# Performance work log

Hardware: AMD Instinct MI355X
Metric: run time of the kernel (lower is better)

The kernel has to match this reference:

```python
import jax, jax.numpy as jnp
import numpy as np

SCALE = 0.08838834764831845  # 1/sqrt(128)

def setup_inputs() -> dict:
    key = jax.random.key(0)
    k1, k2 = jax.random.split(key)
    x1 = jax.random.normal(k1, (16, 2048, 128), dtype=jnp.float32)
    x2 = jax.random.normal(k2, (16, 2048, 128), dtype=jnp.float32)
    return {"x1": x1, "x2": x2}

def reference(x1, x2):
    # qk = x1 @ x2^T  -> [B, Lq, Lk]
    qk = jnp.einsum('bqd,bkd->bqk', x1, x2) * SCALE
    attn = jax.nn.softmax(qk, axis=-1)
    # dropout p=0.0 -> identity
    # output = attn @ x2 (x2 doubles as values in the source module)
    out = jnp.einsum('bqk,bkd->bqd', attn, x2)
    return out
```

## Files before the change

### kernel.cpp

```cpp
#include <hip/hip_runtime.h>
#include <hip/hip_bf16.h>

typedef __attribute__((ext_vector_type(8))) short bf16x8;
typedef __attribute__((ext_vector_type(4))) short bf16x4;
typedef __attribute__((ext_vector_type(4))) float f32x4;

#define NSEQ 2048
#define DH 128
#define QBLK 64
#define KVB 64

#if __has_builtin(__builtin_amdgcn_exp2f)
#define FEXP(x) __builtin_amdgcn_exp2f(x)
#define QSCALE 0.12751743f
#else
#define FEXP(x) __expf(x)
#define QSCALE 0.08838834764831845f
#endif

__device__ __forceinline__ short f2bf(float x) {
  unsigned int u = __float_as_uint(x);
  unsigned int r = (u + 0x7fffu + ((u >> 16) & 1u)) >> 16;
  return (short)r;
}

__device__ __forceinline__ int swzT(int d) {
  return ((d & 7) ^ ((d >> 3) & 7)) << 4;
}

__global__ __launch_bounds__(256, 2) void attn_fwd(
    const float* __restrict__ x1, const float* __restrict__ x2,
    float* __restrict__ out) {
  __shared__ char lds[40960];
  char* kvA = lds;
  char* kvT = lds + 16384;
  char* plds = lds + 32768;

  const int tid = threadIdx.x;
  const int lane = tid & 63;
  const int wid = tid >> 6;
  const int g = lane >> 4;
  const int q15 = lane & 15;

  const int bb = blockIdx.y;
  const int qbase = blockIdx.x * QBLK + wid * 16;

  const float* x1b = x1 + (size_t)bb * NSEQ * DH;
  const float* x2b = x2 + (size_t)bb * NSEQ * DH;

  bf16x8 qf[4];
  {
    const float* qp = x1b + (size_t)(qbase + q15) * DH + g * 8;
#pragma unroll
    for (int c = 0; c < 4; ++c) {
      f32x4 v0 = *(const f32x4*)(qp + c * 32);
      f32x4 v1 = *(const f32x4*)(qp + c * 32 + 4);
      bf16x8 f;
#pragma unroll
      for (int i = 0; i < 4; ++i) {
        f[i] = f2bf(v0[i] * QSCALE);
        f[i + 4] = f2bf(v1[i] * QSCALE);
      }
      qf[c] = f;
    }
  }

  const int kgrp = tid >> 4;
  const int dg = tid & 15;
  f32x4 ra[4][2];

  auto LOADRA = [&](int kv0) {
    if (kv0 < NSEQ) {
#pragma unroll
      for (int p = 0; p < 4; ++p) {
        const float* s = x2b + (size_t)(kv0 + kgrp * 4 + p) * DH + dg * 8;
        ra[p][0] = *(const f32x4*)s;
        ra[p][1] = *(const f32x4*)(s + 4);
      }
    }
  };

  auto WRITELDS = [&]() {
    short sb[4][8];
#pragma unroll
    for (int p = 0; p < 4; ++p)
#pragma unroll
      for (int j = 0; j < 8; ++j) sb[p][j] = f2bf(ra[p][j >> 2][j & 3]);
#pragma unroll
    for (int p = 0; p < 4; ++p) {
      const int key = kgrp * 4 + p;
      bf16x8 pack;
#pragma unroll
      for (int j = 0; j < 8; ++j) pack[j] = sb[p][j];
      *(bf16x8*)(kvA + key * 256 + ((dg * 16) ^ ((key & 7) << 4))) = pack;
    }
#pragma unroll
    for (int i = 0; i < 8; ++i) {
      const int d = dg * 8 + i;
      bf16x4 col;
#pragma unroll
      for (int p = 0; p < 4; ++p) col[p] = sb[p][i];
      *(bf16x4*)(kvT + d * 128 + ((kgrp * 8) ^ swzT(d))) = col;
    }
  };

  float m_run = -1e30f;
  float l_run = 0.f;
  f32x4 o[8];
#pragma unroll
  for (int dc = 0; dc < 8; ++dc) o[dc] = (f32x4){0.f, 0.f, 0.f, 0.f};

  LOADRA(0);
  WRITELDS();
  LOADRA(KVB);
  asm volatile("s_waitcnt lgkmcnt(0)" ::: "memory");
  __builtin_amdgcn_s_barrier();

  for (int kv0 = 0; kv0 < NSEQ; kv0 += KVB) {
    f32x4 sf[4];
#pragma unroll
    for (int kb = 0; kb < 4; ++kb) {
      sf[kb] = (f32x4){0.f, 0.f, 0.f, 0.f};
      const int key = kb * 16 + q15;
#pragma unroll
      for (int c = 0; c < 4; ++c) {
        bf16x8 a = *(const bf16x8*)(kvA + key * 256 +
                                    ((c * 64 + g * 16) ^ ((key & 7) << 4)));
        sf[kb] = __builtin_amdgcn_mfma_f32_16x16x32_bf16(a, qf[c], sf[kb], 0, 0, 0);
      }
    }

    float mloc = -1e30f;
#pragma unroll
    for (int kb = 0; kb < 4; ++kb)
#pragma unroll
      for (int r = 0; r < 4; ++r) mloc = fmaxf(mloc, sf[kb][r]);
    mloc = fmaxf(mloc, __shfl_xor(mloc, 16));
    mloc = fmaxf(mloc, __shfl_xor(mloc, 32));
    const float mnew = fmaxf(m_run, mloc);
    const float corr = FEXP(m_run - mnew);
    float tsum = 0.f;
    short pb[4][4];
#pragma unroll
    for (int kb = 0; kb < 4; ++kb)
#pragma unroll
      for (int r = 0; r < 4; ++r) {
        float pv = FEXP(sf[kb][r] - mnew);
        tsum += pv;
        pb[kb][r] = f2bf(pv);
      }
    tsum += __shfl_xor(tsum, 16);
    tsum += __shfl_xor(tsum, 32);
    l_run = l_run * corr + tsum;
    m_run = mnew;

#pragma unroll
    for (int r = 0; r < 4; ++r) {
      const float fr = __shfl(corr, g * 4 + r);
#pragma unroll
      for (int dc = 0; dc < 8; ++dc) o[dc][r] *= fr;
    }

#pragma unroll
    for (int kb = 0; kb < 4; ++kb) {
      bf16x4 pk;
#pragma unroll
      for (int r = 0; r < 4; ++r) pk[r] = pb[kb][r];
      *(bf16x4*)(plds + wid * 2048 + q15 * 128 +
                 ((kb * 32 + g * 8) ^ ((q15 & 7) << 4))) = pk;
    }

#pragma unroll
    for (int kc = 0; kc < 2; ++kc) {
      bf16x8 pa = *(const bf16x8*)(plds + wid * 2048 + q15 * 128 +
                                   ((kc * 64 + g * 16) ^ ((q15 & 7) << 4)));
#pragma unroll
      for (int dc = 0; dc < 8; ++dc) {
        const int d = dc * 16 + q15;
        bf16x8 vb = *(const bf16x8*)(kvT + d * 128 +
                                     ((kc * 64 + g * 16) ^ swzT(d)));
        o[dc] = __builtin_amdgcn_mfma_f32_16x16x32_bf16(pa, vb, o[dc], 0, 0, 0);
      }
    }

    if (kv0 + KVB < NSEQ) {
      __syncthreads();
      WRITELDS();
      LOADRA(kv0 + 2 * KVB);
      asm volatile("s_waitcnt lgkmcnt(0)" ::: "memory");
      __builtin_amdgcn_s_barrier();
    }
  }

#pragma unroll
  for (int r = 0; r < 4; ++r) {
    const float linv = 1.0f / __shfl(l_run, g * 4 + r);
    const int q = qbase + g * 4 + r;
    float* op = out + (size_t)bb * NSEQ * DH + (size_t)q * DH + q15;
#pragma unroll
    for (int dc = 0; dc < 8; ++dc) op[dc * 16] = o[dc][r] * linv;
  }
}

extern "C" void kernel_launch(void* const* d_in, const int* in_sizes, int n_in,
                              void* d_out, int out_size, void* d_ws, size_t ws_size,
                              hipStream_t stream) {
  const float* x1 = (const float*)d_in[0];
  const float* x2 = (const float*)d_in[1];
  float* out = (float*)d_out;
  dim3 grid(NSEQ / QBLK, 16);
  attn_fwd<<<grid, dim3(256), 0, stream>>>(x1, x2, out);
}
```

Before: 148.2 us.

## Double-buffer K/V LDS tiles, defer softmax rescale, use packed bf16 converts

Doubles the LDS K/V buffers so the next tile's conversion and store run during the current tile's compute, leaving one barrier per iteration instead of a full sync plus barrier. Skips the online-softmax rescale of the accumulator unless the running max grows by more than a threshold (log2 domain). Replaces the manual bf16 rounding with the hardware v_cvt_pk_bf16_f32 instruction. LDS use grows to 72KB per block, which may limit blocks per CU. The deferred rescale lets unnormalised exponentials reach up to 2^8, which stays within float range.

New measurement: 134.4 us. -9.3%, faster.

```diff
diff --git a/kernel.cpp b/kernel.cpp
--- a/kernel.cpp
+++ b/kernel.cpp
@@ -2,27 +2,24 @@
 #include <hip/hip_bf16.h>
 
 typedef __attribute__((ext_vector_type(8))) short bf16x8;
-typedef __attribute__((ext_vector_type(4))) short bf16x4;
 typedef __attribute__((ext_vector_type(4))) float f32x4;
+typedef __attribute__((ext_vector_type(4))) unsigned u32x4;
+typedef __attribute__((ext_vector_type(2))) unsigned u32x2;
 
 #define NSEQ 2048
 #define DH 128
 #define QBLK 64
 #define KVB 64
-
-#if __has_builtin(__builtin_amdgcn_exp2f)
-#define FEXP(x) __builtin_amdgcn_exp2f(x)
-#define QSCALE 0.12751743f
-#else
-#define FEXP(x) __expf(x)
-#define QSCALE 0.08838834764831845f
-#endif
-
-__device__ __forceinline__ short f2bf(float x) {
-  unsigned int u = __float_as_uint(x);
-  unsigned int r = (u + 0x7fffu + ((u >> 16) & 1u)) >> 16;
-  return (short)r;
-}
+#define QSCALE 0.12751744716167933f
+#define DEFER_THR 8.0f
+#define KVSTRIDE 32768
+
+__device__ __forceinline__ unsigned cvtpk(float lo, float hi) {
+  unsigned r;
+  asm("v_cvt_pk_bf16_f32 %0, %1, %2" : "=v"(r) : "v"(lo), "v"(hi));
+  return r;
+}
+__device__ __forceinline__ float fexp2(float x) { return __builtin_amdgcn_exp2f(x); }
 
 __device__ __forceinline__ int swzT(int d) {
   return ((d & 7) ^ ((d >> 3) & 7)) << 4;
@@ -31,10 +28,8 @@
 __global__ __launch_bounds__(256, 2) void attn_fwd(
     const float* __restrict__ x1, const float* __restrict__ x2,
     float* __restrict__ out) {
-  __shared__ char lds[40960];
-  char* kvA = lds;
-  char* kvT = lds + 16384;
-  char* plds = lds + 32768;
+  __shared__ char lds[73728];
+  char* plds = lds + 65536;
 
   const int tid = threadIdx.x;
   const int lane = tid & 63;
@@ -48,20 +43,19 @@
   const float* x1b = x1 + (size_t)bb * NSEQ * DH;
   const float* x2b = x2 + (size_t)bb * NSEQ * DH;
 
-  bf16x8 qf[4];
+  u32x4 qf[4];
   {
     const float* qp = x1b + (size_t)(qbase + q15) * DH + g * 8;
 #pragma unroll
     for (int c = 0; c < 4; ++c) {
       f32x4 v0 = *(const f32x4*)(qp + c * 32);
       f32x4 v1 = *(const f32x4*)(qp + c * 32 + 4);
-      bf16x8 f;
-#pragma unroll
-      for (int i = 0; i < 4; ++i) {
-        f[i] = f2bf(v0[i] * QSCALE);
-        f[i + 4] = f2bf(v1[i] * QSCALE);
-      }
-      qf[c] = f;
+      u32x4 w;
+      w[0] = cvtpk(v0[0] * QSCALE, v0[1] * QSCALE);
+      w[1] = cvtpk(v0[2] * QSCALE, v0[3] * QSCALE);
+      w[2] = cvtpk(v1[0] * QSCALE, v1[1] * QSCALE);
+      w[3] = cvtpk(v1[2] * QSCALE, v1[3] * QSCALE);
+      qf[c] = w;
     }
   }
 
@@ -80,28 +74,29 @@
     }
   };
 
-  auto WRITELDS = [&]() {
-    short sb[4][8];
-#pragma unroll
-    for (int p = 0; p < 4; ++p)
-#pragma unroll
-      for (int j = 0; j < 8; ++j) sb[p][j] = f2bf(ra[p][j >> 2][j & 3]);
+  auto WRITELDS = [&](int b) {
+    char* kvAb = lds + b * KVSTRIDE;
+    char* kvTb = kvAb + 16384;
 #pragma unroll
     for (int p = 0; p < 4; ++p) {
+      u32x4 w;
+      w[0] = cvtpk(ra[p][0][0], ra[p][0][1]);
+      w[1] = cvtpk(ra[p][0][2], ra[p][0][3]);
+      w[2] = cvtpk(ra[p][1][0], ra[p][1][1]);
+      w[3] = cvtpk(ra[p][1][2], ra[p][1][3]);
       const int key = kgrp * 4 + p;
-      bf16x8 pack;
-#pragma unroll
-      for (int j = 0; j < 8; ++j) pack[j] = sb[p][j];
-      *(bf16x8*)(kvA + key * 256 + ((dg * 16) ^ ((key & 7) << 4))) = pack;
-    }
-#pragma unroll
-    for (int i = 0; i < 8; ++i) {
-      const int d = dg * 8 + i;
-      bf16x4 col;
-#pragma unroll
-      for (int p = 0; p < 4; ++p) col[p] = sb[p][i];
-      *(bf16x4*)(kvT + d * 128 + ((kgrp * 8) ^ swzT(d))) = col;
-    }
+      *(u32x4*)(kvAb + key * 256 + ((dg * 16) ^ ((key & 7) << 4))) = w;
+    }
+#pragma unroll
+    for (int h = 0; h < 2; ++h)
+#pragma unroll
+      for (int ii = 0; ii < 4; ++ii) {
+        const int d = dg * 8 + h * 4 + ii;
+        u32x2 cw;
+        cw[0] = cvtpk(ra[0][h][ii], ra[1][h][ii]);
+        cw[1] = cvtpk(ra[2][h][ii], ra[3][h][ii]);
+        *(u32x2*)(kvTb + d * 128 + ((kgrp * 8) ^ swzT(d))) = cw;
+      }
   };
 
   float m_run = -1e30f;
@@ -111,12 +106,16 @@
   for (int dc = 0; dc < 8; ++dc) o[dc] = (f32x4){0.f, 0.f, 0.f, 0.f};
 
   LOADRA(0);
-  WRITELDS();
+  WRITELDS(0);
   LOADRA(KVB);
   asm volatile("s_waitcnt lgkmcnt(0)" ::: "memory");
   __builtin_amdgcn_s_barrier();
+  int cur = 0;
 
   for (int kv0 = 0; kv0 < NSEQ; kv0 += KVB) {
+    char* kvA = lds + cur * KVSTRIDE;
+    char* kvT = kvA + 16384;
+
     f32x4 sf[4];
 #pragma unroll
     for (int kb = 0; kb < 4; ++kb) {
@@ -126,7 +125,8 @@
       for (int c = 0; c < 4; ++c) {
         bf16x8 a = *(const bf16x8*)(kvA + key * 256 +
                                     ((c * 64 + g * 16) ^ ((key & 7) << 4)));
-        sf[kb] = __builtin_amdgcn_mfma_f32_16x16x32_bf16(a, qf[c], sf[kb], 0, 0, 0);
+        sf[kb] = __builtin_amdgcn_mfma_f32_16x16x32_bf16(
+            a, *(const bf16x8*)&qf[c], sf[kb], 0, 0, 0);
       }
     }
 
@@ -137,37 +137,44 @@
       for (int r = 0; r < 4; ++r) mloc = fmaxf(mloc, sf[kb][r]);
     mloc = fmaxf(mloc, __shfl_xor(mloc, 16));
     mloc = fmaxf(mloc, __shfl_xor(mloc, 32));
-    const float mnew = fmaxf(m_run, mloc);
-    const float corr = FEXP(m_run - mnew);
+    if (!__all(mloc <= m_run + DEFER_THR)) {
+      const float mnew = fmaxf(m_run, mloc);
+      const float corr = fexp2(m_run - mnew);
+#pragma unroll
+      for (int r = 0; r < 4; ++r) {
+        const float fr = __shfl(corr, g * 4 + r);
+#pragma unroll
+        for (int dc = 0; dc < 8; ++dc) o[dc][r] *= fr;
+      }
+      l_run *= corr;
+      m_run = mnew;
+    }
     float tsum = 0.f;
-    short pb[4][4];
+    float pf[4][4];
 #pragma unroll
     for (int kb = 0; kb < 4; ++kb)
 #pragma unroll
       for (int r = 0; r < 4; ++r) {
-        float pv = FEXP(sf[kb][r] - mnew);
+        const float pv = fexp2(sf[kb][r] - m_run);
         tsum += pv;
-        pb[kb][r] = f2bf(pv);
+        pf[kb][r] = pv;
       }
     tsum += __shfl_xor(tsum, 16);
     tsum += __shfl_xor(tsum, 32);
-    l_run = l_run * corr + tsum;
-    m_run = mnew;
-
-#pragma unroll
-    for (int r = 0; r < 4; ++r) {
-      const float fr = __shfl(corr, g * 4 + r);
-#pragma unroll
-      for (int dc = 0; dc < 8; ++dc) o[dc][r] *= fr;
+    l_run += tsum;
+
+    if (kv0 + KVB < NSEQ) {
+      WRITELDS(cur ^ 1);
+      LOADRA(kv0 + 2 * KVB);
     }
 
 #pragma unroll
     for (int kb = 0; kb < 4; ++kb) {
-      bf16x4 pk;
-#pragma unroll
-      for (int r = 0; r < 4; ++r) pk[r] = pb[kb][r];
-      *(bf16x4*)(plds + wid * 2048 + q15 * 128 +
-                 ((kb * 32 + g * 8) ^ ((q15 & 7) << 4))) = pk;
+      u32x2 pw;
+      pw[0] = cvtpk(pf[kb][0], pf[kb][1]);
+      pw[1] = cvtpk(pf[kb][2], pf[kb][3]);
+      *(u32x2*)(plds + wid * 2048 + q15 * 128 +
+                ((kb * 32 + g * 8) ^ ((q15 & 7) << 4))) = pw;
     }
 
 #pragma unroll
@@ -183,13 +190,9 @@
       }
     }
 
-    if (kv0 + KVB < NSEQ) {
-      __syncthreads();
-      WRITELDS();
-      LOADRA(kv0 + 2 * KVB);
-      asm volatile("s_waitcnt lgkmcnt(0)" ::: "memory");
-      __builtin_amdgcn_s_barrier();
-    }
+    asm volatile("s_waitcnt lgkmcnt(0)" ::: "memory");
+    __builtin_amdgcn_s_barrier();
+    cur ^= 1;
   }
 
 #pragma unroll
```
